# Kernel optimization log

Measured on AMD Instinct MI355X. Metric: run time of the kernel, lower is better.

Reference implementation:

```python
import jax, jax.numpy as jnp
import numpy as np

N = 50000
E = 800000
D = 64

def setup_inputs() -> dict:
    key = jax.random.key(0)
    k1, k2, k3, k4 = jax.random.split(key, 4)
    node_features = jax.random.normal(k1, (N, D), dtype=jnp.float32)
    edge_index = jax.random.randint(k2, (E, 2), 0, N, dtype=jnp.int64)
    W = jax.random.normal(k3, (D, D), dtype=jnp.float32) * (1.0 / np.sqrt(D))
    b_lin = jax.random.normal(k4, (D,), dtype=jnp.float32) * 0.02
    bias = jnp.zeros((D,), dtype=jnp.float32)
    return {"node_features": node_features, "edge_index": edge_index,
            "W": W, "b_lin": b_lin, "bias": bias}

def reference(node_features, edge_index, W, b_lin, bias):
    # linear: [N, D_in] @ [D_in, D_out]
    x = node_features @ W.T + b_lin
    src = edge_index[:, 0]
    dst = edge_index[:, 1]
    n = x.shape[0]
    # scatter-add of gathered source features into destination nodes
    aggregated = jax.ops.segment_sum(x[src], dst, num_segments=n)
    degree = jax.ops.segment_sum(jnp.ones((src.shape[0],), x.dtype), dst,
                                 num_segments=n)
    degree = jnp.maximum(degree, 1.0)
    x = x + aggregated / degree[:, None]
    return jax.nn.relu(x + bias)
```

## Files before the change

### kernel.cpp

```cpp
#include <hip/hip_runtime.h>
#include <hip/hip_bf16.h>

#define NN 50000
#define DD 64
#define EE 800000
#define NTILE 3125
#define BCAP 64
#define NSB 782
#define NLB 782

typedef unsigned short u16;
typedef unsigned int u32;
typedef __attribute__((ext_vector_type(8))) short bf16x8;
typedef __attribute__((ext_vector_type(4))) float f32x4;

__device__ __forceinline__ float bf2f(u16 u) {
  u32 t = ((u32)u) << 16;
  return __builtin_bit_cast(float, t);
}
__device__ __forceinline__ u16 f2bf(float f) {
  u32 b = __builtin_bit_cast(u32, f);
  u32 r = (b + 0x7FFF + ((b >> 16) & 1)) >> 16;
  return (u16)r;
}

__global__ __launch_bounds__(256) void fused_ls_kernel(
    const float* __restrict__ nf, const int* __restrict__ ei,
    const float* __restrict__ W, const float* __restrict__ b_lin,
    u16* __restrict__ x16, u16* __restrict__ bucket, int* __restrict__ cnt) {
  __shared__ u16 Wsh[64 * 72];
  int b = blockIdx.x;
  int tid = threadIdx.x;

  if (b < NSB) {
    int e0 = (b * 256 + tid) * 4;
    if (e0 >= EE) return;
    int4 pa = *(const int4*)(ei + 2 * e0);
    int4 pb = *(const int4*)(ei + 2 * e0 + 4);
    int p0 = atomicAdd(&cnt[pa.y], 1);
    int p1 = atomicAdd(&cnt[pa.w], 1);
    int p2 = atomicAdd(&cnt[pb.y], 1);
    int p3 = atomicAdd(&cnt[pb.w], 1);
    if (p0 < BCAP) bucket[pa.y * BCAP + p0] = (u16)pa.x;
    if (p1 < BCAP) bucket[pa.w * BCAP + p1] = (u16)pa.z;
    if (p2 < BCAP) bucket[pb.y * BCAP + p2] = (u16)pb.x;
    if (p3 < BCAP) bucket[pb.w * BCAP + p3] = (u16)pb.z;
    return;
  }

#pragma unroll
  for (int s = 0; s < 16; ++s) {
    int idx = s * 256 + tid;
    Wsh[(idx >> 6) * 72 + (idx & 63)] = f2bf(W[idx]);
  }
  __syncthreads();

  int wave = tid >> 6;
  int lane = tid & 63;
  int tile = (b - NSB) * 4 + wave;
  if (tile >= NTILE) return;

  int m = lane & 15;
  int quad = lane >> 4;
  int rowbase = tile * 16;

  bf16x8 bfrag[4][2];
#pragma unroll
  for (int c = 0; c < 4; ++c) {
#pragma unroll
    for (int ks = 0; ks < 2; ++ks) {
      const u16* p = &Wsh[(c * 16 + m) * 72 + ks * 32 + quad * 8];
      bfrag[c][ks] = *(const bf16x8*)p;
    }
  }

  bf16x8 afrag[2];
#pragma unroll
  for (int ks = 0; ks < 2; ++ks) {
    const float* p = nf + (rowbase + m) * DD + ks * 32 + quad * 8;
    float4 lo = *(const float4*)p;
    float4 hi = *(const float4*)(p + 4);
    bf16x8 a;
    a[0] = (short)f2bf(lo.x); a[1] = (short)f2bf(lo.y);
    a[2] = (short)f2bf(lo.z); a[3] = (short)f2bf(lo.w);
    a[4] = (short)f2bf(hi.x); a[5] = (short)f2bf(hi.y);
    a[6] = (short)f2bf(hi.z); a[7] = (short)f2bf(hi.w);
    afrag[ks] = a;
  }

  f32x4 acc[4];
#pragma unroll
  for (int c = 0; c < 4; ++c) {
    acc[c][0] = 0.0f; acc[c][1] = 0.0f; acc[c][2] = 0.0f; acc[c][3] = 0.0f;
  }
#pragma unroll
  for (int c = 0; c < 4; ++c) {
    acc[c] = __builtin_amdgcn_mfma_f32_16x16x32_bf16(afrag[0], bfrag[c][0], acc[c], 0, 0, 0);
    acc[c] = __builtin_amdgcn_mfma_f32_16x16x32_bf16(afrag[1], bfrag[c][1], acc[c], 0, 0, 0);
  }

#pragma unroll
  for (int c = 0; c < 4; ++c) {
    int gcol = c * 16 + m;
    float bl = b_lin[gcol];
#pragma unroll
    for (int r2 = 0; r2 < 4; ++r2) {
      int grow = rowbase + quad * 4 + r2;
      x16[grow * DD + gcol] = f2bf(acc[c][r2] + bl);
    }
  }
}

template <int BASE, int LEN>
__device__ __forceinline__ float chunkN(int my, int n,
                                        const u16* __restrict__ x16, int j) {
  float v[LEN];
#pragma unroll
  for (int k = 0; k < LEN; ++k) {
    int s = __builtin_amdgcn_readlane(my, BASE + k);
    v[k] = bf2f(x16[s * DD + j]);
  }
  float a = 0.0f;
#pragma unroll
  for (int k = 0; k < LEN; ++k) a += (BASE + k < n) ? v[k] : 0.0f;
  return a;
}

__global__ __launch_bounds__(256) void gather_kernel(
    const u16* __restrict__ x16, const u16* __restrict__ bucket,
    const int* __restrict__ cnt, const float* __restrict__ bias,
    float* __restrict__ out) {
  int i = blockIdx.x * 4 + (threadIdx.x >> 6);
  int j = threadIdx.x & 63;
  int deg = cnt[i];
  int win = deg < BCAP ? deg : BCAP;
  int my = (int)bucket[i * BCAP + j];

  float acc = chunkN<0, 16>(my, win, x16, j);
  if (win > 16) acc += chunkN<16, 8>(my, win, x16, j);
  if (win > 24) acc += chunkN<24, 8>(my, win, x16, j);
  if (win > 32) acc += chunkN<32, 8>(my, win, x16, j);
  if (win > 40) acc += chunkN<40, 8>(my, win, x16, j);
  if (win > 48) acc += chunkN<48, 8>(my, win, x16, j);
  if (win > 56) acc += chunkN<56, 8>(my, win, x16, j);

  float inv = 1.0f / fmaxf((float)deg, 1.0f);
  float self = bf2f(x16[i * DD + j]);
  out[i * DD + j] = fmaxf(fmaf(acc, inv, self + bias[j]), 0.0f);
}

extern "C" void kernel_launch(void* const* d_in, const int* in_sizes, int n_in,
                              void* d_out, int out_size, void* d_ws, size_t ws_size,
                              hipStream_t stream) {
  const float* nf    = (const float*)d_in[0];
  const int*   ei    = (const int*)d_in[1];
  const float* W     = (const float*)d_in[2];
  const float* b_lin = (const float*)d_in[3];
  const float* bias  = (const float*)d_in[4];
  float* out = (float*)d_out;

  u16* x16    = (u16*)d_ws;
  u16* bucket = x16 + (size_t)NN * DD;
  int* cnt    = (int*)(bucket + (size_t)NN * BCAP);

  hipMemsetAsync(cnt, 0, NN * sizeof(int), stream);
  fused_ls_kernel<<<NSB + NLB, 256, 0, stream>>>(nf, ei, W, b_lin, x16, bucket, cnt);
  gather_kernel<<<NN / 4, 256, 0, stream>>>(x16, bucket, cnt, bias, out);
}
```

Before: 142.6 us.

## Replace global-atomic bucketing with two-pass radix partition by destination range

Global atomics on per-node counters for bucketing are replaced by a partitioning pipeline. Per-chunk histograms of 256-node destination ranges are built in shared memory, a single-block scan turns them into offsets, and the edges are partitioned into range-contiguous packed records. Each bucket block then builds its 256 nodes' buckets in LDS and writes them out coalesced. This removes contended global atomics, scattered 2-byte writes and the memset, but adds three kernel launches, a serial single-block scan and an extra pass over the edges.

```diff
diff --git a/kernel.cpp b/kernel.cpp
--- a/kernel.cpp
+++ b/kernel.cpp
@@ -6,7 +6,10 @@
 #define EE 800000
 #define NTILE 3125
 #define BCAP 64
-#define NSB 782
+#define NR 196
+#define NPB 512
+#define EPB 1563
+#define NCB 512
 #define NLB 782
 
 typedef unsigned short u16;
@@ -24,30 +27,34 @@
   return (u16)r;
 }
 
-__global__ __launch_bounds__(256) void fused_ls_kernel(
+__device__ __forceinline__ int chunk_of(int b) { return (b & 7) * 64 + (b >> 3); }
+
+__global__ __launch_bounds__(256) void fused_lc_kernel(
     const float* __restrict__ nf, const int* __restrict__ ei,
     const float* __restrict__ W, const float* __restrict__ b_lin,
-    u16* __restrict__ x16, u16* __restrict__ bucket, int* __restrict__ cnt) {
-  __shared__ u16 Wsh[64 * 72];
+    u16* __restrict__ x16, int* __restrict__ cnts) {
   int b = blockIdx.x;
   int tid = threadIdx.x;
 
-  if (b < NSB) {
-    int e0 = (b * 256 + tid) * 4;
-    if (e0 >= EE) return;
-    int4 pa = *(const int4*)(ei + 2 * e0);
-    int4 pb = *(const int4*)(ei + 2 * e0 + 4);
-    int p0 = atomicAdd(&cnt[pa.y], 1);
-    int p1 = atomicAdd(&cnt[pa.w], 1);
-    int p2 = atomicAdd(&cnt[pb.y], 1);
-    int p3 = atomicAdd(&cnt[pb.w], 1);
-    if (p0 < BCAP) bucket[pa.y * BCAP + p0] = (u16)pa.x;
-    if (p1 < BCAP) bucket[pa.w * BCAP + p1] = (u16)pa.z;
-    if (p2 < BCAP) bucket[pb.y * BCAP + p2] = (u16)pb.x;
-    if (p3 < BCAP) bucket[pb.w * BCAP + p3] = (u16)pb.z;
+  if (b < NCB) {
+    __shared__ int csh[NR];
+    int cb = chunk_of(b);
+    int ebeg = cb * EPB;
+    int eend = ebeg + EPB;
+    if (eend > EE) eend = EE;
+    if (tid < NR) csh[tid] = 0;
+    __syncthreads();
+#pragma unroll 1
+    for (int i = ebeg + tid; i < eend; i += 256) {
+      int2 v = *(const int2*)(ei + 2 * i);
+      atomicAdd(&csh[v.y >> 8], 1);
+    }
+    __syncthreads();
+    if (tid < NR) cnts[cb * NR + tid] = csh[tid];
     return;
   }
 
+  __shared__ u16 Wsh[64 * 72];
 #pragma unroll
   for (int s = 0; s < 16; ++s) {
     int idx = s * 256 + tid;
@@ -57,7 +64,7 @@
 
   int wave = tid >> 6;
   int lane = tid & 63;
-  int tile = (b - NSB) * 4 + wave;
+  int tile = (b - NCB) * 4 + wave;
   if (tile >= NTILE) return;
 
   int m = lane & 15;
@@ -111,6 +118,93 @@
   }
 }
 
+__global__ __launch_bounds__(256) void scan_kernel(
+    const int* __restrict__ cnts, int* __restrict__ offs,
+    int* __restrict__ range_base) {
+  __shared__ int sp[256];
+  int t = threadIdx.x;
+  int run = 0;
+  if (t < NR) {
+#pragma unroll 4
+    for (int b = 0; b < NPB; ++b) {
+      int v = cnts[b * NR + t];
+      offs[b * NR + t] = run;
+      run += v;
+    }
+  }
+  sp[t] = (t < NR) ? run : 0;
+  __syncthreads();
+#pragma unroll
+  for (int o = 1; o < 256; o <<= 1) {
+    int u = (t >= o) ? sp[t - o] : 0;
+    __syncthreads();
+    sp[t] += u;
+    __syncthreads();
+  }
+  int base = (t > 0) ? sp[t - 1] : 0;
+  if (t < NR) {
+    range_base[t] = base;
+    if (t == NR - 1) range_base[NR] = base + run;
+#pragma unroll 4
+    for (int b = 0; b < NPB; ++b) offs[b * NR + t] += base;
+  }
+}
+
+__global__ __launch_bounds__(256) void part_kernel(
+    const int* __restrict__ ei, const int* __restrict__ offs,
+    u32* __restrict__ part) {
+  __shared__ int off_sh[NR];
+  __shared__ int lcnt[NR];
+  int b = blockIdx.x;
+  int tid = threadIdx.x;
+  int cb = chunk_of(b);
+  if (tid < NR) {
+    off_sh[tid] = offs[cb * NR + tid];
+    lcnt[tid] = 0;
+  }
+  __syncthreads();
+  int ebeg = cb * EPB;
+  int eend = ebeg + EPB;
+  if (eend > EE) eend = EE;
+#pragma unroll 1
+  for (int i = ebeg + tid; i < eend; i += 256) {
+    int2 v = *(const int2*)(ei + 2 * i);
+    int r = v.y >> 8;
+    int lp = atomicAdd(&lcnt[r], 1);
+    part[off_sh[r] + lp] = (u32)v.x | (((u32)v.y & 255u) << 16);
+  }
+}
+
+__global__ __launch_bounds__(256) void bucket_kernel(
+    const u32* __restrict__ part, const int* __restrict__ range_base,
+    u16* __restrict__ bucket, int* __restrict__ cnt) {
+  __shared__ u16 bkt[256 * BCAP];
+  __shared__ int lcnt[256];
+  int r = blockIdx.x;
+  int tid = threadIdx.x;
+  lcnt[tid] = 0;
+  __syncthreads();
+  int beg = range_base[r];
+  int end = range_base[r + 1];
+#pragma unroll 1
+  for (int i = beg + tid; i < end; i += 256) {
+    u32 e = part[i];
+    int dl = (int)(e >> 16);
+    int lp = atomicAdd(&lcnt[dl], 1);
+    if (lp < BCAP) bkt[dl * BCAP + lp] = (u16)(e & 0xFFFFu);
+  }
+  __syncthreads();
+  int nb = r << 8;
+  if (nb + tid < NN) cnt[nb + tid] = lcnt[tid];
+  const u32* bs = (const u32*)bkt;
+  u32* bg = (u32*)bucket;
+#pragma unroll 1
+  for (int k = tid; k < 256 * (BCAP / 2); k += 256) {
+    int dl = k >> 5;
+    if (nb + dl < NN) bg[(size_t)(nb + dl) * (BCAP / 2) + (k & 31)] = bs[k];
+  }
+}
+
 template <int BASE, int LEN>
 __device__ __forceinline__ float chunkN(int my, int n,
                                         const u16* __restrict__ x16, int j) {
@@ -159,11 +253,17 @@
   const float* bias  = (const float*)d_in[4];
   float* out = (float*)d_out;
 
-  u16* x16    = (u16*)d_ws;
-  u16* bucket = x16 + (size_t)NN * DD;
-  int* cnt    = (int*)(bucket + (size_t)NN * BCAP);
-
-  hipMemsetAsync(cnt, 0, NN * sizeof(int), stream);
-  fused_ls_kernel<<<NSB + NLB, 256, 0, stream>>>(nf, ei, W, b_lin, x16, bucket, cnt);
+  u16* x16        = (u16*)d_ws;
+  u16* bucket     = x16 + (size_t)NN * DD;
+  int* cnt        = (int*)(bucket + (size_t)NN * BCAP);
+  u32* part       = (u32*)(cnt + NN);
+  int* cnts       = (int*)(part + EE);
+  int* offs       = cnts + NPB * NR;
+  int* range_base = offs + NPB * NR;
+
+  fused_lc_kernel<<<NCB + NLB, 256, 0, stream>>>(nf, ei, W, b_lin, x16, cnts);
+  scan_kernel<<<1, 256, 0, stream>>>(cnts, offs, range_base);
+  part_kernel<<<NPB, 256, 0, stream>>>(ei, offs, part);
+  bucket_kernel<<<NR, 256, 0, stream>>>(part, range_base, bucket, cnt);
   gather_kernel<<<NN / 4, 256, 0, stream>>>(x16, bucket, cnt, bias, out);
 }
```

Result: slower. 217.4 us (+52.4%).

## Replace global-atomic edge bucketing with two-pass partitioned binning in shared memory

Applied to the files above, without the earlier changes.

Edges are first binned by destination range (256 nodes) per block using shared-memory atomics into fixed-capacity cells, then a second kernel per range builds per-node buckets in shared memory and writes them out coalesced. This removes the global atomic counters and the memset. In exchange it adds a kernel launch, about 12.8 MB of extra intermediate traffic, and a low-occupancy bucketing pass. Edges are dropped if any cell exceeds 32 entries, which changes the degree in that case.

```diff
diff --git a/kernel.cpp b/kernel.cpp
--- a/kernel.cpp
+++ b/kernel.cpp
@@ -6,7 +6,10 @@
 #define EE 800000
 #define NTILE 3125
 #define BCAP 64
-#define NSB 782
+#define NR 196
+#define NPB 512
+#define EPB 1563
+#define CCAP 32
 #define NLB 782
 
 typedef unsigned short u16;
@@ -24,27 +27,35 @@
   return (u16)r;
 }
 
-__global__ __launch_bounds__(256) void fused_ls_kernel(
+__global__ __launch_bounds__(256) void fused_pl_kernel(
     const float* __restrict__ nf, const int* __restrict__ ei,
     const float* __restrict__ W, const float* __restrict__ b_lin,
-    u16* __restrict__ x16, u16* __restrict__ bucket, int* __restrict__ cnt) {
+    u16* __restrict__ x16, u32* __restrict__ pcell, int* __restrict__ ccnt) {
   __shared__ u16 Wsh[64 * 72];
+  __shared__ int lcnt[NR];
   int b = blockIdx.x;
   int tid = threadIdx.x;
 
-  if (b < NSB) {
-    int e0 = (b * 256 + tid) * 4;
-    if (e0 >= EE) return;
-    int4 pa = *(const int4*)(ei + 2 * e0);
-    int4 pb = *(const int4*)(ei + 2 * e0 + 4);
-    int p0 = atomicAdd(&cnt[pa.y], 1);
-    int p1 = atomicAdd(&cnt[pa.w], 1);
-    int p2 = atomicAdd(&cnt[pb.y], 1);
-    int p3 = atomicAdd(&cnt[pb.w], 1);
-    if (p0 < BCAP) bucket[pa.y * BCAP + p0] = (u16)pa.x;
-    if (p1 < BCAP) bucket[pa.w * BCAP + p1] = (u16)pa.z;
-    if (p2 < BCAP) bucket[pb.y * BCAP + p2] = (u16)pb.x;
-    if (p3 < BCAP) bucket[pb.w * BCAP + p3] = (u16)pb.z;
+  if (b < NPB) {
+    if (tid < NR) lcnt[tid] = 0;
+    __syncthreads();
+    int ebeg = b * EPB;
+    int eend = ebeg + EPB;
+    if (eend > EE) eend = EE;
+#pragma unroll 1
+    for (int i = ebeg + tid; i < eend; i += 256) {
+      int2 v = *(const int2*)(ei + 2 * i);
+      int r = v.y >> 8;
+      int lp = atomicAdd(&lcnt[r], 1);
+      if (lp < CCAP)
+        pcell[((size_t)r * NPB + b) * CCAP + lp] =
+            (u32)v.x | (((u32)v.y & 255u) << 16);
+    }
+    __syncthreads();
+    if (tid < NR) {
+      int c = lcnt[tid];
+      ccnt[tid * NPB + b] = c < CCAP ? c : CCAP;
+    }
     return;
   }
 
@@ -57,7 +68,7 @@
 
   int wave = tid >> 6;
   int lane = tid & 63;
-  int tile = (b - NSB) * 4 + wave;
+  int tile = (b - NPB) * 4 + wave;
   if (tile >= NTILE) return;
 
   int m = lane & 15;
@@ -111,6 +122,44 @@
   }
 }
 
+__global__ __launch_bounds__(256) void bucket_kernel(
+    const u32* __restrict__ pcell, const int* __restrict__ ccnt,
+    u16* __restrict__ bucket, int* __restrict__ cnt) {
+  __shared__ u16 bkt[256 * BCAP];
+  __shared__ int lcnt[256];
+  __shared__ int ccnt_sh[NPB];
+  int r = blockIdx.x;
+  int tid = threadIdx.x;
+  lcnt[tid] = 0;
+  ccnt_sh[tid] = ccnt[r * NPB + tid];
+  ccnt_sh[tid + 256] = ccnt[r * NPB + tid + 256];
+  __syncthreads();
+
+  const u32* pr = pcell + (size_t)r * NPB * CCAP;
+#pragma unroll 1
+  for (int k = tid; k < NPB * CCAP; k += 256) {
+    u32 e = pr[k];
+    int cb = k >> 5;
+    int slot = k & 31;
+    if (slot < ccnt_sh[cb]) {
+      int dl = (int)(e >> 16);
+      int lp = atomicAdd(&lcnt[dl], 1);
+      if (lp < BCAP) bkt[dl * BCAP + lp] = (u16)(e & 0xFFFFu);
+    }
+  }
+  __syncthreads();
+
+  int nb = r << 8;
+  if (nb + tid < NN) cnt[nb + tid] = lcnt[tid];
+  const u32* bs = (const u32*)bkt;
+  u32* bg = (u32*)bucket;
+#pragma unroll 1
+  for (int k = tid; k < 256 * (BCAP / 2); k += 256) {
+    int dl = k >> 5;
+    if (nb + dl < NN) bg[(size_t)(nb + dl) * (BCAP / 2) + (k & 31)] = bs[k];
+  }
+}
+
 template <int BASE, int LEN>
 __device__ __forceinline__ float chunkN(int my, int n,
                                         const u16* __restrict__ x16, int j) {
@@ -162,8 +211,10 @@
   u16* x16    = (u16*)d_ws;
   u16* bucket = x16 + (size_t)NN * DD;
   int* cnt    = (int*)(bucket + (size_t)NN * BCAP);
-
-  hipMemsetAsync(cnt, 0, NN * sizeof(int), stream);
-  fused_ls_kernel<<<NSB + NLB, 256, 0, stream>>>(nf, ei, W, b_lin, x16, bucket, cnt);
+  u32* pcell  = (u32*)(cnt + NN);
+  int* ccnt   = (int*)(pcell + (size_t)NR * NPB * CCAP);
+
+  fused_pl_kernel<<<NPB + NLB, 256, 0, stream>>>(nf, ei, W, b_lin, x16, pcell, ccnt);
+  bucket_kernel<<<NR, 256, 0, stream>>>(pcell, ccnt, bucket, cnt);
   gather_kernel<<<NN / 4, 256, 0, stream>>>(x16, bucket, cnt, bias, out);
 }
```

New measurement: 128.9 us. 9.6% less time.
